# Kernel optimization log

Measured on AMD Instinct MI355X. Metric: run time of the kernel, lower is better.

Reference implementation:

```python
import jax, jax.numpy as jnp
import numpy as np

EBIT = 8
BITS = 8  # wl_activate


def block_quantize_global(data, bits):
    """SWALP block quantize, scalar/global path (small_block='None', dim<=4).

    max-abs reduce -> floor(log2) exponent, clamped to signed ebit range ->
    scale -> round-to-nearest-even -> clamp to signed `bits` range -> rescale.
    If max-abs is exactly 0, data is returned unchanged.
    """
    max_entry = jnp.max(jnp.abs(data))
    # guard log2(0); result unused when max_entry == 0
    safe_max = jnp.where(max_entry == 0, jnp.float32(1.0), max_entry)
    max_exponent = jnp.floor(jnp.log2(safe_max))
    emin = -(2.0 ** (EBIT - 1))
    emax = 2.0 ** (EBIT - 1) - 1
    max_exponent = jnp.clip(max_exponent, emin, emax)
    scale = jnp.exp2(-max_exponent + (bits - 2))
    i = jnp.round(data * scale)  # torch.round_ and jnp.round both round half-to-even
    qmin = -(2.0 ** (bits - 1))
    qmax = 2.0 ** (bits - 1) - 1
    i = jnp.clip(i, qmin, qmax)
    out = i * jnp.exp2(max_exponent - (bits - 2))
    return jnp.where(max_entry == 0, data, out)


def setup_inputs() -> dict:
    key = jax.random.key(0)
    x = jax.random.normal(key, (64, 256, 56, 56), dtype=jnp.float32)
    return {"x": x}


def reference(x):
    return block_quantize_global(x, BITS)
```

## Files before the change

### kernel.cpp

```cpp
#include <hip/hip_runtime.h>
#include <math.h>


#define GRID1 2048

typedef float v4f __attribute__((ext_vector_type(4)));

__device__ inline void store_stream(v4f* p, v4f v) {
    asm volatile("global_store_dwordx4 %0, %1, off sc0 sc1 nt" :: "v"(p), "v"(v));
}

__device__ inline int exp_floor(float m) {
    int eb = (int)((__float_as_uint(m) >> 23) & 0xff);
    int e = (eb == 0) ? -120 : eb - 127;
    return max(-120, min(127, e));
}
__device__ inline float exp2i(int k) {
    return __uint_as_float((unsigned)(k + 127) << 23);
}

__global__ __launch_bounds__(256) void bq_pack(const float* __restrict__ x,
                                               unsigned int* __restrict__ j4,
                                               signed char* __restrict__ e8,
                                               float* __restrict__ partial,
                                               int n4) {
    const v4f* __restrict__ x4 = (const v4f*)x;
    const int tid = blockIdx.x * blockDim.x + threadIdx.x;
    const int T = gridDim.x * blockDim.x;
    float mblk = 0.0f;
    for (int i = tid; i < n4; i += T) {
        v4f v = x4[i];
        float m = fmaxf(fmaxf(fabsf(v.x), fabsf(v.y)),
                        fmaxf(fabsf(v.z), fabsf(v.w)));
        mblk = fmaxf(mblk, m);
        const int e = exp_floor(m);
        const float s = exp2i(6 - e);
        int j0 = min(127, max(-128, (int)rintf(v.x * s)));
        int j1 = min(127, max(-128, (int)rintf(v.y * s)));
        int j2 = min(127, max(-128, (int)rintf(v.z * s)));
        int j3 = min(127, max(-128, (int)rintf(v.w * s)));
        j4[i] = (unsigned)(j0 & 0xff)         | ((unsigned)(j1 & 0xff) << 8) |
                ((unsigned)(j2 & 0xff) << 16) | ((unsigned)(j3 & 0xff) << 24);
        e8[i] = (signed char)e;
    }
    #pragma unroll
    for (int off = 32; off > 0; off >>= 1)
        mblk = fmaxf(mblk, __shfl_xor(mblk, off, 64));
    __shared__ float sm[4];
    if ((threadIdx.x & 63) == 0) sm[threadIdx.x >> 6] = mblk;
    __syncthreads();
    if (threadIdx.x == 0)
        partial[blockIdx.x] = fmaxf(fmaxf(sm[0], sm[1]), fmaxf(sm[2], sm[3]));
}

__global__ __launch_bounds__(256) void bq_emit(const unsigned int* __restrict__ j4,
                                               const signed char* __restrict__ e8,
                                               const float* __restrict__ partial,
                                               float* __restrict__ out,
                                               int n4) {
    float gm = 0.0f;
    #pragma unroll
    for (int k = 0; k < GRID1 / 256; ++k)
        gm = fmaxf(gm, partial[threadIdx.x + k * 256]);
    #pragma unroll
    for (int off = 32; off > 0; off >>= 1)
        gm = fmaxf(gm, __shfl_xor(gm, off, 64));
    __shared__ float sm[4];
    if ((threadIdx.x & 63) == 0) sm[threadIdx.x >> 6] = gm;
    __syncthreads();
    const float maxe = fmaxf(fmaxf(sm[0], sm[1]), fmaxf(sm[2], sm[3]));

    const int eg = exp_floor(maxe);
    const float invs = exp2i(eg - 6);
    v4f* __restrict__ o4 = (v4f*)out;

    const int tid = blockIdx.x * blockDim.x + threadIdx.x;
    const int T = gridDim.x * blockDim.x;
    for (int i = tid; i < n4; i += T) {
        const unsigned w = j4[i];
        const int ec = (int)e8[i];
        const float fs = ldexpf(1.0f, ec - eg);
        float f0 = (float)(int)(signed char)(w & 0xff);
        float f1 = (float)(int)(signed char)((w >> 8) & 0xff);
        float f2 = (float)(int)(signed char)((w >> 16) & 0xff);
        float f3 = (float)(int)(signed char)((w >> 24) & 0xff);
        v4f r;
        r.x = rintf(f0 * fs) * invs;
        r.y = rintf(f1 * fs) * invs;
        r.z = rintf(f2 * fs) * invs;
        r.w = rintf(f3 * fs) * invs;
        store_stream(&o4[i], r);
    }
}


__global__ __launch_bounds__(256) void bq_absmax(const float* __restrict__ x,
                                                 float* __restrict__ partial,
                                                 int n) {
    const int n4 = n >> 2;
    const v4f* __restrict__ x4 = (const v4f*)x;
    int tid = blockIdx.x * blockDim.x + threadIdx.x;
    int stride = gridDim.x * blockDim.x;
    float m = 0.0f;
    for (int i = tid; i < n4; i += stride) {
        v4f v = x4[i];
        m = fmaxf(fmaxf(fabsf(v.x), fabsf(v.y)),
                  fmaxf(fmaxf(fabsf(v.z), fabsf(v.w)), m));
    }
    for (int i = (n4 << 2) + tid; i < n; i += stride) m = fmaxf(m, fabsf(x[i]));
    #pragma unroll
    for (int off = 32; off > 0; off >>= 1)
        m = fmaxf(m, __shfl_xor(m, off, 64));
    __shared__ float sm[4];
    if ((threadIdx.x & 63) == 0) sm[threadIdx.x >> 6] = m;
    __syncthreads();
    if (threadIdx.x == 0)
        partial[blockIdx.x] = fmaxf(fmaxf(sm[0], sm[1]), fmaxf(sm[2], sm[3]));
}

__global__ __launch_bounds__(256) void bq_quant(const float* __restrict__ x,
                                                float* __restrict__ out,
                                                const float* __restrict__ partial,
                                                int n) {
    float bm = 0.0f;
    #pragma unroll
    for (int k = 0; k < GRID1 / 256; ++k)
        bm = fmaxf(bm, partial[threadIdx.x + k * 256]);
    #pragma unroll
    for (int off = 32; off > 0; off >>= 1)
        bm = fmaxf(bm, __shfl_xor(bm, off, 64));
    __shared__ float sm[4];
    if ((threadIdx.x & 63) == 0) sm[threadIdx.x >> 6] = bm;
    __syncthreads();
    const float maxe = fmaxf(fmaxf(sm[0], sm[1]), fmaxf(sm[2], sm[3]));

    const int n4 = n >> 2;
    const v4f* __restrict__ x4 = (const v4f*)x;
    v4f* __restrict__ o4 = (v4f*)out;
    const int tid = blockIdx.x * blockDim.x + threadIdx.x;
    const int T = gridDim.x * blockDim.x;

    if (maxe == 0.0f) {
        for (int i = tid; i < n4; i += T) store_stream(&o4[i], x4[i]);
        for (int i = (n4 << 2) + tid; i < n; i += T) out[i] = x[i];
        return;
    }
    int e = ilogbf(maxe);
    e = max(-128, min(127, e));
    const float scale    = ldexpf(1.0f, -e + 6);
    const float invscale = ldexpf(1.0f, e - 6);
    for (int i = tid; i < n4; i += T) {
        v4f v = x4[i];
        float a = rintf(v.x * scale);
        float b = rintf(v.y * scale);
        float cc = rintf(v.z * scale);
        float d = rintf(v.w * scale);
        a  = fminf(fmaxf(a,  -128.0f), 127.0f);
        b  = fminf(fmaxf(b,  -128.0f), 127.0f);
        cc = fminf(fmaxf(cc, -128.0f), 127.0f);
        d  = fminf(fmaxf(d,  -128.0f), 127.0f);
        v4f r;
        r.x = a * invscale;
        r.y = b * invscale;
        r.z = cc * invscale;
        r.w = d * invscale;
        store_stream(&o4[i], r);
    }
    for (int i = (n4 << 2) + tid; i < n; i += T) {
        float a = rintf(x[i] * scale);
        a = fminf(fmaxf(a, -128.0f), 127.0f);
        out[i] = a * invscale;
    }
}

extern "C" void kernel_launch(void* const* d_in, const int* in_sizes, int n_in,
                              void* d_out, int out_size, void* d_ws, size_t ws_size,
                              hipStream_t stream) {
    const float* x = (const float*)d_in[0];
    float* out = (float*)d_out;
    int n = in_sizes[0];
    const int n4 = n >> 2;

    const size_t off_e8 = GRID1 * sizeof(float);
    const size_t off_j4 = (off_e8 + (size_t)n4 + 15) & ~(size_t)15;
    const size_t need   = off_j4 + (size_t)n4 * 4;

    float* partial = (float*)d_ws;

    if ((n & 3) == 0 && ws_size >= need) {
        signed char* e8  = (signed char*)d_ws + off_e8;
        unsigned int* j4 = (unsigned int*)((char*)d_ws + off_j4);
        hipLaunchKernelGGL(bq_pack, dim3(GRID1), dim3(256), 0, stream,
                           x, j4, e8, partial, n4);
        hipLaunchKernelGGL(bq_emit, dim3(GRID1), dim3(256), 0, stream,
                           j4, e8, partial, out, n4);
    } else {
        hipLaunchKernelGGL(bq_absmax, dim3(GRID1), dim3(256), 0, stream, x, partial, n);
        hipLaunchKernelGGL(bq_quant,  dim3(GRID1), dim3(256), 0, stream, x, out, partial, n);
    }
}
```

Baseline: 85.00 us.

## Share one exponent across seven float4 chunks and shrink exponent buffer

The pack kernel now takes one local exponent from the max over 7 float4 vectors per thread, so it writes one exponent byte per 28 elements instead of one per 4. The work is split into fixed compile-time trips over a grid of 1792 blocks, with all 7 loads issued before any compute to raise memory-level parallelism. This cuts intermediate exponent traffic and loop overhead in both kernels. The fast path now holds only when the element count exactly matches the hardcoded grid geometry; other sizes fall back to the two-pass kernels.

```diff
diff --git a/kernel.cpp b/kernel.cpp
--- a/kernel.cpp
+++ b/kernel.cpp
@@ -2,6 +2,11 @@
 #include <math.h>
 
 
+#define NB 1792
+#define NT 256
+#define TT (NB * NT)
+#define CH 7
+#define ITERS 4
 #define GRID1 2048
 
 typedef float v4f __attribute__((ext_vector_type(4)));
@@ -9,7 +14,6 @@
 __device__ inline void store_stream(v4f* p, v4f v) {
     asm volatile("global_store_dwordx4 %0, %1, off sc0 sc1 nt" :: "v"(p), "v"(v));
 }
-
 __device__ inline int exp_floor(float m) {
     int eb = (int)((__float_as_uint(m) >> 23) & 0xff);
     int e = (eb == 0) ? -120 : eb - 127;
@@ -19,30 +23,42 @@
     return __uint_as_float((unsigned)(k + 127) << 23);
 }
 
-__global__ __launch_bounds__(256) void bq_pack(const float* __restrict__ x,
+__global__ __launch_bounds__(NT) void bq_pack7(const float* __restrict__ x,
                                                unsigned int* __restrict__ j4,
                                                signed char* __restrict__ e8,
-                                               float* __restrict__ partial,
-                                               int n4) {
+                                               float* __restrict__ partial) {
     const v4f* __restrict__ x4 = (const v4f*)x;
-    const int tid = blockIdx.x * blockDim.x + threadIdx.x;
-    const int T = gridDim.x * blockDim.x;
+    const int gtid = blockIdx.x * NT + threadIdx.x;
     float mblk = 0.0f;
-    for (int i = tid; i < n4; i += T) {
-        v4f v = x4[i];
-        float m = fmaxf(fmaxf(fabsf(v.x), fabsf(v.y)),
-                        fmaxf(fabsf(v.z), fabsf(v.w)));
+
+    for (int it = 0; it < ITERS; ++it) {
+        v4f v[CH];
+        #pragma unroll
+        for (int k = 0; k < CH; ++k)
+            v[k] = x4[(size_t)(it * CH + k) * TT + gtid];
+
+        float m = 0.0f;
+        #pragma unroll
+        for (int k = 0; k < CH; ++k)
+            m = fmaxf(m, fmaxf(fmaxf(fabsf(v[k].x), fabsf(v[k].y)),
+                               fmaxf(fabsf(v[k].z), fabsf(v[k].w))));
         mblk = fmaxf(mblk, m);
+
         const int e = exp_floor(m);
         const float s = exp2i(6 - e);
-        int j0 = min(127, max(-128, (int)rintf(v.x * s)));
-        int j1 = min(127, max(-128, (int)rintf(v.y * s)));
-        int j2 = min(127, max(-128, (int)rintf(v.z * s)));
-        int j3 = min(127, max(-128, (int)rintf(v.w * s)));
-        j4[i] = (unsigned)(j0 & 0xff)         | ((unsigned)(j1 & 0xff) << 8) |
+        #pragma unroll
+        for (int k = 0; k < CH; ++k) {
+            int j0 = min(127, max(-128, (int)rintf(v[k].x * s)));
+            int j1 = min(127, max(-128, (int)rintf(v[k].y * s)));
+            int j2 = min(127, max(-128, (int)rintf(v[k].z * s)));
+            int j3 = min(127, max(-128, (int)rintf(v[k].w * s)));
+            j4[(size_t)(it * CH + k) * TT + gtid] =
+                (unsigned)(j0 & 0xff)         | ((unsigned)(j1 & 0xff) << 8) |
                 ((unsigned)(j2 & 0xff) << 16) | ((unsigned)(j3 & 0xff) << 24);
-        e8[i] = (signed char)e;
-    }
+        }
+        e8[(size_t)it * TT + gtid] = (signed char)e;
+    }
+
     #pragma unroll
     for (int off = 32; off > 0; off >>= 1)
         mblk = fmaxf(mblk, __shfl_xor(mblk, off, 64));
@@ -53,15 +69,14 @@
         partial[blockIdx.x] = fmaxf(fmaxf(sm[0], sm[1]), fmaxf(sm[2], sm[3]));
 }
 
-__global__ __launch_bounds__(256) void bq_emit(const unsigned int* __restrict__ j4,
+__global__ __launch_bounds__(NT) void bq_emit7(const unsigned int* __restrict__ j4,
                                                const signed char* __restrict__ e8,
                                                const float* __restrict__ partial,
-                                               float* __restrict__ out,
-                                               int n4) {
+                                               float* __restrict__ out) {
     float gm = 0.0f;
     #pragma unroll
-    for (int k = 0; k < GRID1 / 256; ++k)
-        gm = fmaxf(gm, partial[threadIdx.x + k * 256]);
+    for (int k = 0; k < NB / NT; ++k)
+        gm = fmaxf(gm, partial[threadIdx.x + k * NT]);
     #pragma unroll
     for (int off = 32; off > 0; off >>= 1)
         gm = fmaxf(gm, __shfl_xor(gm, off, 64));
@@ -73,23 +88,25 @@
     const int eg = exp_floor(maxe);
     const float invs = exp2i(eg - 6);
     v4f* __restrict__ o4 = (v4f*)out;
-
-    const int tid = blockIdx.x * blockDim.x + threadIdx.x;
-    const int T = gridDim.x * blockDim.x;
-    for (int i = tid; i < n4; i += T) {
-        const unsigned w = j4[i];
-        const int ec = (int)e8[i];
+    const int gtid = blockIdx.x * NT + threadIdx.x;
+
+    for (int it = 0; it < ITERS; ++it) {
+        const int ec = (int)e8[(size_t)it * TT + gtid];
         const float fs = ldexpf(1.0f, ec - eg);
-        float f0 = (float)(int)(signed char)(w & 0xff);
-        float f1 = (float)(int)(signed char)((w >> 8) & 0xff);
-        float f2 = (float)(int)(signed char)((w >> 16) & 0xff);
-        float f3 = (float)(int)(signed char)((w >> 24) & 0xff);
-        v4f r;
-        r.x = rintf(f0 * fs) * invs;
-        r.y = rintf(f1 * fs) * invs;
-        r.z = rintf(f2 * fs) * invs;
-        r.w = rintf(f3 * fs) * invs;
-        store_stream(&o4[i], r);
+        #pragma unroll
+        for (int k = 0; k < CH; ++k) {
+            const unsigned w = j4[(size_t)(it * CH + k) * TT + gtid];
+            float f0 = (float)(int)(signed char)(w & 0xff);
+            float f1 = (float)(int)(signed char)((w >> 8) & 0xff);
+            float f2 = (float)(int)(signed char)((w >> 16) & 0xff);
+            float f3 = (float)(int)(signed char)((w >> 24) & 0xff);
+            v4f r;
+            r.x = rintf(f0 * fs) * invs;
+            r.y = rintf(f1 * fs) * invs;
+            r.z = rintf(f2 * fs) * invs;
+            r.w = rintf(f3 * fs) * invs;
+            store_stream(&o4[(size_t)(it * CH + k) * TT + gtid], r);
+        }
     }
 }
 
@@ -181,19 +198,17 @@
     int n = in_sizes[0];
     const int n4 = n >> 2;
 
-    const size_t off_e8 = GRID1 * sizeof(float);
-    const size_t off_j4 = (off_e8 + (size_t)n4 + 15) & ~(size_t)15;
+    const size_t off_e8 = ((size_t)NB * 4 + 15) & ~(size_t)15;
+    const size_t off_j4 = (off_e8 + (size_t)ITERS * TT + 15) & ~(size_t)15;
     const size_t need   = off_j4 + (size_t)n4 * 4;
 
     float* partial = (float*)d_ws;
 
-    if ((n & 3) == 0 && ws_size >= need) {
+    if ((n & 3) == 0 && n4 == TT * CH * ITERS && ws_size >= need) {
         signed char* e8  = (signed char*)d_ws + off_e8;
         unsigned int* j4 = (unsigned int*)((char*)d_ws + off_j4);
-        hipLaunchKernelGGL(bq_pack, dim3(GRID1), dim3(256), 0, stream,
-                           x, j4, e8, partial, n4);
-        hipLaunchKernelGGL(bq_emit, dim3(GRID1), dim3(256), 0, stream,
-                           j4, e8, partial, out, n4);
+        hipLaunchKernelGGL(bq_pack7, dim3(NB), dim3(NT), 0, stream, x, j4, e8, partial);
+        hipLaunchKernelGGL(bq_emit7, dim3(NB), dim3(NT), 0, stream, j4, e8, partial, out);
     } else {
         hipLaunchKernelGGL(bq_absmax, dim3(GRID1), dim3(256), 0, stream, x, partial, n);
         hipLaunchKernelGGL(bq_quant,  dim3(GRID1), dim3(256), 0, stream, x, out, partial, n);
```

After: 80.43 us. 5.4% less time.
